# Optimization experiments

Hardware: AMD Instinct MI355X
Metric: run time of the kernel (lower is better)

The kernel has to match this reference:

```python
import jax, jax.numpy as jnp
import numpy as np

B, T = 64, 256
CHAR_V, CHAR_D = 8000, 128
WORD_V, WORD_D = 100000, 300
POS_V, POS_D = 30, 64
SPO_D = 20
D = CHAR_D + WORD_D + POS_D + SPO_D  # 512
L, H, KD, VD, INNER = 4, 8, 64, 64, 2048
C = 25  # num tag classes


def _layer_norm(x, g, b, eps=1e-5):
    m = jnp.mean(x, axis=-1, keepdims=True)
    v = jnp.mean(jnp.square(x - m), axis=-1, keepdims=True)
    return (x - m) * jax.lax.rsqrt(v + eps) * g + b


def setup_inputs() -> dict:
    key = jax.random.key(0)
    ks = jax.random.split(key, 40)
    s = 0.05
    n = lambda k, shp, sc=0.05: jax.random.normal(k, shp, jnp.float32) * sc
    return {
        "char": jax.random.randint(ks[0], (B, T), 0, CHAR_V),
        "word": jax.random.randint(ks[1], (B, T), 0, WORD_V),
        "pos": jax.random.randint(ks[2], (B, T), 0, POS_V),
        "spo": jax.random.normal(ks[3], (B, SPO_D), jnp.float32),
        "seq_len": jax.random.randint(ks[4], (B,), 1, T + 1),
        "tag": jax.random.randint(ks[5], (B, T), 0, C),
        "char_table": n(ks[6], (CHAR_V, CHAR_D)),
        "word_table": n(ks[7], (WORD_V, WORD_D)),
        "pos_table": n(ks[8], (POS_V, POS_D)),
        "ln0_g": jnp.ones((D,), jnp.float32),
        "ln0_b": jnp.zeros((D,), jnp.float32),
        "Wq": n(ks[9], (L, D, H * KD)), "bq": jnp.zeros((L, H * KD), jnp.float32),
        "Wk": n(ks[10], (L, D, H * KD)), "bk": jnp.zeros((L, H * KD), jnp.float32),
        "Wv": n(ks[11], (L, D, H * VD)), "bv": jnp.zeros((L, H * VD), jnp.float32),
        "Wo": n(ks[12], (L, H * VD, D)), "bo": jnp.zeros((L, D), jnp.float32),
        "ln1_g": jnp.ones((L, D), jnp.float32), "ln1_b": jnp.zeros((L, D), jnp.float32),
        "W1": n(ks[13], (L, D, INNER)), "b1": jnp.zeros((L, INNER), jnp.float32),
        "W2": n(ks[14], (L, INNER, D)), "b2": jnp.zeros((L, D), jnp.float32),
        "ln2_g": jnp.ones((L, D), jnp.float32), "ln2_b": jnp.zeros((L, D), jnp.float32),
        "Wout": n(ks[15], (D, C)), "bout": jnp.zeros((C,), jnp.float32),
        "trans": n(ks[16], (C, C)),
    }


def _forward(spo, char_table, word_table, pos_table, ln0_g, ln0_b,
             Wq, bq, Wk, bk, Wv, bv, Wo, bo, ln1_g, ln1_b,
             W1, b1, W2, b2, ln2_g, ln2_b, Wout, bout, trans,
             char, word, pos, seq_len, tag):
    # mask[b,t] = t < seq_len[b]
    mask = (jnp.arange(T)[None, :] < seq_len[:, None]).astype(jnp.float32)  # [B,T]

    # embed + concat + layernorm (dropout in eval mode = identity)
    x = jnp.concatenate([
        char_table[char], word_table[word], pos_table[pos],
        jnp.broadcast_to(spo[:, None, :], (B, T, SPO_D)),
    ], axis=-1)  # [B,T,D]
    x = _layer_norm(x, ln0_g, ln0_b)

    neg_inf = jnp.finfo(x.dtype).min
    key_ok = mask[:, None, None, :] > 0  # [B,1,1,T] key padding mask
    scale = jnp.sqrt(jnp.asarray(KD, x.dtype))
    for l in range(L):
        q = (x @ Wq[l] + bq[l]).reshape(B, T, H, KD).transpose(0, 2, 1, 3)
        k = (x @ Wk[l] + bk[l]).reshape(B, T, H, KD).transpose(0, 2, 1, 3)
        v = (x @ Wv[l] + bv[l]).reshape(B, T, H, VD).transpose(0, 2, 1, 3)
        scores = jnp.einsum('bhqd,bhkd->bhqk', q, k) / scale
        scores = jnp.where(key_ok, scores, neg_inf)
        attn = jax.nn.softmax(scores, axis=-1)
        ctx = jnp.einsum('bhqk,bhkd->bhqd', attn, v).transpose(0, 2, 1, 3).reshape(B, T, H * VD)
        att_out = ctx @ Wo[l] + bo[l]
        h1 = _layer_norm(att_out + x, ln1_g[l], ln1_b[l])
        ff = jax.nn.relu(h1 @ W1[l] + b1[l]) @ W2[l] + b2[l]
        x = _layer_norm(ff + h1, ln2_g[l], ln2_b[l]) * mask[:, :, None]

    logits = x @ Wout + bout  # [B,T,C]

    # ---- CRF negative log likelihood (include_start_end_trans=False) ----
    lg = logits.transpose(1, 0, 2)  # [T,B,C]
    m = mask.T                      # [T,B]

    def step(alpha, inp):
        emit, mt = inp  # emit [B,C], mt [B]
        tmp = alpha[:, :, None] + trans[None, :, :] + emit[:, None, :]  # [B,C,C]
        new = jax.nn.logsumexp(tmp, axis=1)
        alpha = jnp.where(mt[:, None] > 0, new, alpha)
        return alpha, None

    alpha, _ = jax.lax.scan(step, lg[0], (lg[1:], m[1:]))
    log_z = jax.nn.logsumexp(alpha, axis=-1)  # [B]

    tags_t = tag.T  # [T,B]
    emit_gold = jnp.take_along_axis(lg, tags_t[:, :, None], axis=-1)[..., 0] * m  # [T,B]
    trans_gold = trans[tags_t[:-1], tags_t[1:]] * m[1:]  # [T-1,B]
    gold = emit_gold.sum(0) + trans_gold.sum(0)  # [B]

    return jnp.mean(log_z - gold)


def reference(char, word, pos, spo, seq_len, tag, char_table, word_table, pos_table,
              ln0_g, ln0_b, Wq, bq, Wk, bk, Wv, bv, Wo, bo, ln1_g, ln1_b,
              W1, b1, W2, b2, ln2_g, ln2_b, Wout, bout, trans):
    return _forward(spo, char_table, word_table, pos_table, ln0_g, ln0_b,
                    Wq, bq, Wk, bk, Wv, bv, Wo, bo, ln1_g, ln1_b,
                    W1, b1, W2, b2, ln2_g, ln2_b, Wout, bout, trans,
                    char, word, pos, seq_len, tag)
```

## Files before the change

kernel.cpp:

```cpp
#include <hip/hip_runtime.h>
#include <cmath>

namespace {

constexpr int LT = 4;
constexpr int BB = 64;
constexpr int TT = 256;
constexpr int DD = 512;
constexpr int HH = 8;
constexpr int DH = 64;
constexpr int FF = 2048;
constexpr int CC = 25;
constexpr int M_ALL = BB * TT;
constexpr size_t MB = 1024 * 1024;

typedef __attribute__((ext_vector_type(8))) short short8;
typedef __attribute__((ext_vector_type(4))) short short4_;
typedef __attribute__((ext_vector_type(4))) float f32x4;
typedef __attribute__((ext_vector_type(4))) _Float16 half4;

__device__ __forceinline__ float b2f(unsigned short u) {
  union { unsigned int i; float f; } x; x.i = ((unsigned int)u) << 16; return x.f;
}
__device__ __forceinline__ unsigned short f2b(float f) {
  union { float f; unsigned int i; } x; x.f = f;
  unsigned int r = x.i + 0x7FFFu + ((x.i >> 16) & 1u);
  return (unsigned short)(r >> 16);
}
__device__ __forceinline__ float rdlane(float v, int l) {
  union { float f; unsigned int i; } x; x.f = v;
  x.i = (unsigned int)__builtin_amdgcn_readlane((int)x.i, l);
  return x.f;
}
__device__ __forceinline__ void gl_lds16(const void* g, void* l) {
  __builtin_amdgcn_global_load_lds(
      (const __attribute__((address_space(1))) unsigned int*)g,
      (__attribute__((address_space(3))) unsigned int*)l, 16, 0, 0);
}
__device__ __forceinline__ float wredsum(float v) {
#pragma unroll
  for (int o = 32; o > 0; o >>= 1) v += __shfl_xor(v, o, 64);
  return v;
}

__global__ __launch_bounds__(64) void prefix_k(const int* __restrict__ sl,
                                               int* __restrict__ boff) {
  const int l = threadIdx.x;
  int s = sl[l];
#pragma unroll
  for (int o = 1; o < 64; o <<= 1) {
    const int u = __shfl_up(s, o, 64);
    if (l >= o) s += u;
  }
  boff[l + 1] = s;
  if (l == 0) boff[0] = 0;
}

__global__ __launch_bounds__(256) void rowmap_k(const int* __restrict__ sl,
                                                const int* __restrict__ boff,
                                                int* __restrict__ rowmap) {
  const int b = blockIdx.x, t = threadIdx.x;
  if (t < sl[b]) rowmap[boff[b] + t] = (b << 8) | t;
}

__global__ __launch_bounds__(256) void wconv_k(const float* __restrict__ in,
                                               unsigned short* __restrict__ out,
                                               int K, int N, size_t lstride) {
  __shared__ float ts[64][65];
  const int k0 = blockIdx.x * 64, n0 = blockIdx.y * 64;
  in += (size_t)blockIdx.z * K * N;
  out += (size_t)blockIdx.z * lstride;
  const int tid = threadIdx.x;
  for (int i = tid; i < 1024; i += 256) {
    const int r = i >> 4, c4 = i & 15;
    const float4 f = *(const float4*)&in[(size_t)(k0 + r) * N + n0 + c4 * 4];
    ts[r][c4 * 4 + 0] = f.x; ts[r][c4 * 4 + 1] = f.y;
    ts[r][c4 * 4 + 2] = f.z; ts[r][c4 * 4 + 3] = f.w;
  }
  __syncthreads();
  const int n_r = tid >> 2, kc = (tid & 3) * 16;
  short8 v0, v1;
#pragma unroll
  for (int j = 0; j < 8; ++j) {
    v0[j] = (short)f2b(ts[kc + j][n_r]);
    v1[j] = (short)f2b(ts[kc + 8 + j][n_r]);
  }
  unsigned short* op = out + (size_t)(n0 + n_r) * K + k0 + kc;
  *(short8*)op = v0;
  *(short8*)(op + 8) = v1;
}

__global__ __launch_bounds__(256) void embed_ln0_k(
    const int* __restrict__ ch, const int* __restrict__ wd, const int* __restrict__ ps,
    const float* __restrict__ spo, const float* __restrict__ ctab,
    const float* __restrict__ wtab, const float* __restrict__ ptab,
    const float* __restrict__ g, const float* __restrict__ be,
    const int* __restrict__ sl, const int* __restrict__ boff,
    unsigned short* __restrict__ xc) {
  const int row = blockIdx.x * 4 + (threadIdx.x >> 6);
  const int b = row >> 8, t = row & 255;
  if (t >= sl[b]) return;
  const int orow = boff[b] + t;
  const int lane = threadIdx.x & 63;
  const int ci = ch[row], wi = wd[row], pi = ps[row];
  float v[8];
#pragma unroll
  for (int j = 0; j < 2; ++j) {
    const int d = j * 256 + lane * 4;
    float4 f;
    if (d < 128)      f = *(const float4*)&ctab[(size_t)ci * 128 + d];
    else if (d < 428) f = *(const float4*)&wtab[(size_t)wi * 300 + (d - 128)];
    else if (d < 492) f = *(const float4*)&ptab[(size_t)pi * 64 + (d - 428)];
    else              f = *(const float4*)&spo[(size_t)b * 20 + (d - 492)];
    v[j * 4 + 0] = f.x; v[j * 4 + 1] = f.y; v[j * 4 + 2] = f.z; v[j * 4 + 3] = f.w;
  }
  float s = 0.f;
#pragma unroll
  for (int i = 0; i < 8; ++i) s += v[i];
  const float mean = wredsum(s) * (1.0f / 512.0f);
  float vs = 0.f;
#pragma unroll
  for (int i = 0; i < 8; ++i) { const float d = v[i] - mean; vs += d * d; }
  const float rstd = rsqrtf(wredsum(vs) * (1.0f / 512.0f) + 1e-5f);
#pragma unroll
  for (int j = 0; j < 2; ++j) {
    const int d = j * 256 + lane * 4;
    const float4 gv = *(const float4*)&g[d];
    const float4 bv = *(const float4*)&be[d];
    short4_ ob;
    ob[0] = (short)f2b((v[j * 4 + 0] - mean) * rstd * gv.x + bv.x);
    ob[1] = (short)f2b((v[j * 4 + 1] - mean) * rstd * gv.y + bv.y);
    ob[2] = (short)f2b((v[j * 4 + 2] - mean) * rstd * gv.z + bv.z);
    ob[3] = (short)f2b((v[j * 4 + 3] - mean) * rstd * gv.w + bv.w);
    *(short4_*)&xc[(size_t)orow * DD + d] = ob;
  }
}

template <int EPI>
__global__ __launch_bounds__(256) void gemm_mfma(
    const unsigned short* __restrict__ A, const unsigned short* __restrict__ Bt,
    const float* __restrict__ bias, const float* __restrict__ bias2,
    const float* __restrict__ bias3, const unsigned short* __restrict__ res,
    const int* __restrict__ Mptr, const int* __restrict__ rowmap,
    void* __restrict__ outv, void* __restrict__ out2v, void* __restrict__ out3v,
    int M, int N, int K) {
  const int Mp = Mptr[0];
  const int m0 = blockIdx.y * 128, n0 = blockIdx.x * 128;
  if (m0 >= Mp) return;
  __shared__ unsigned short As[2][128 * 64];
  __shared__ unsigned short Bs[2][128 * 64];
  const int tid = threadIdx.x;
  const int wid = tid >> 6, lane = tid & 63;
  const int wr = wid >> 1, wc = wid & 1;
  const int cl = lane & 15, rg = lane >> 4;
  f32x4 acc[4][4];
#pragma unroll
  for (int i = 0; i < 4; ++i)
#pragma unroll
    for (int j = 0; j < 4; ++j) acc[i][j] = (f32x4){0.f, 0.f, 0.f, 0.f};

  const int rbase = tid >> 3, sl = tid & 7;
  const int sc = 8 * (sl ^ (rbase & 7));

  auto stage = [&](int buf, int k0) {
#pragma unroll
    for (int i = 0; i < 4; ++i) {
      const int r = i * 32 + rbase;
      gl_lds16(A + (size_t)(m0 + r) * K + k0 + sc,
               (char*)As[buf] + (i * 256 + tid) * 16);
      gl_lds16(Bt + (size_t)(n0 + r) * K + k0 + sc,
               (char*)Bs[buf] + (i * 256 + tid) * 16);
    }
  };

  stage(0, 0);
  __syncthreads();
  int cur = 0;
  for (int k0 = 0; k0 < K; k0 += 64) {
    if (k0 + 64 < K) stage(cur ^ 1, k0 + 64);
#pragma unroll
    for (int ks = 0; ks < 2; ++ks) {
      short8 a[4], b[4];
      const int kbyte = ks * 64 + rg * 16;
#pragma unroll
      for (int f = 0; f < 4; ++f) {
        const int am = wr * 64 + f * 16 + cl;
        a[f] = *(const short8*)((const char*)As[cur] + am * 128 +
                                (kbyte ^ ((am & 7) << 4)));
        const int bn = wc * 64 + f * 16 + cl;
        b[f] = *(const short8*)((const char*)Bs[cur] + bn * 128 +
                                (kbyte ^ ((bn & 7) << 4)));
      }
#pragma unroll
      for (int mi = 0; mi < 4; ++mi)
#pragma unroll
        for (int ni = 0; ni < 4; ++ni)
          acc[mi][ni] = __builtin_amdgcn_mfma_f32_16x16x32_bf16(a[mi], b[ni],
                                                                acc[mi][ni], 0, 0, 0);
    }
    __syncthreads();
    cur ^= 1;
  }

  int rm[4][4];
  if constexpr (EPI == 5) {
#pragma unroll
    for (int mi = 0; mi < 4; ++mi) {
      const int mb_ = m0 + wr * 64 + mi * 16 + rg * 4;
#pragma unroll
      for (int i = 0; i < 4; ++i)
        rm[mi][i] = (mb_ + i < Mp) ? rowmap[mb_ + i] : -1;
    }
  }

#pragma unroll
  for (int ni = 0; ni < 4; ++ni) {
    const int n = n0 + wc * 64 + ni * 16 + cl;
    float bv;
    if constexpr (EPI == 5) {
      bv = (n < 512) ? bias[n] : (n < 1024 ? bias2[n - 512] : bias3[n - 1024]);
    } else {
      bv = bias[n];
    }
#pragma unroll
    for (int mi = 0; mi < 4; ++mi) {
      if constexpr (EPI == 5) {
        const int hh = (n >> 6) & 7, d = n & 63;
        if (n < 1024) {
          unsigned short* outp = (unsigned short*)((n < 512) ? outv : out2v);
#pragma unroll
          for (int i = 0; i < 4; ++i) {
            const int rmv = rm[mi][i];
            if (rmv >= 0) {
              const int bb = rmv >> 8, tt = rmv & 255;
              outp[(((size_t)(bb * HH + hh) * TT + tt) << 6) + d] =
                  f2b(acc[mi][ni][i] + bv);
            }
          }
        } else {
          const int rm0 = rm[mi][0];
          if (rm0 >= 0 && rm[mi][3] == rm0 + 3) {
            half4 pk;
#pragma unroll
            for (int i = 0; i < 4; ++i) pk[i] = (_Float16)(acc[mi][ni][i] + bv);
            *(half4*)((_Float16*)out3v +
                      ((((size_t)((rm0 >> 8) * HH + hh) * DH + d) << 8) + (rm0 & 255))) = pk;
          } else {
#pragma unroll
            for (int i = 0; i < 4; ++i) {
              const int rmv = rm[mi][i];
              if (rmv >= 0)
                ((_Float16*)out3v)[(((size_t)((rmv >> 8) * HH + hh) * DH + d) << 8) +
                                   (rmv & 255)] = (_Float16)(acc[mi][ni][i] + bv);
            }
          }
        }
      } else {
#pragma unroll
        for (int i = 0; i < 4; ++i) {
          const int m = m0 + wr * 64 + mi * 16 + rg * 4 + i;
          const float v = acc[mi][ni][i] + bv;
          if constexpr (EPI == 1) {
            ((unsigned short*)outv)[(size_t)m * N + n] = f2b(fmaxf(v, 0.f));
          } else if constexpr (EPI == 7) {
            ((unsigned short*)outv)[(size_t)m * N + n] =
                f2b(v + b2f(res[(size_t)m * N + n]));
          }
        }
      }
    }
  }
}

__global__ __launch_bounds__(256) void attn_mfma_k(
    const unsigned short* __restrict__ qb, const unsigned short* __restrict__ kbp,
    const _Float16* __restrict__ vtp, const int* __restrict__ seq_len,
    const int* __restrict__ boff, unsigned short* __restrict__ cb) {
  __shared__ unsigned short Ks[256 * 64];
  __shared__ _Float16 Vs[64 * 256];
  __shared__ unsigned short Os[64 * 64];
  const int bh = blockIdx.x;
  const int b = bh >> 3, h = bh & 7;
  const int tid = threadIdx.x;
  const int wid = tid >> 6, lane = tid & 63;
  const int cl = lane & 15, rg = lane >> 4;
  const int len = seq_len[b];
  const int off = boff[b];

  {
    const int r = tid >> 3, sl = tid & 7;
#pragma unroll
    for (int i = 0; i < 8; ++i) {
      if (i * 32 < len) {
        const int row = i * 32 + r;
        gl_lds16(kbp + ((size_t)bh * TT + row) * DH + 8 * (sl ^ (row & 7)),
                 (char*)Ks + (i * 256 + tid) * 16);
      }
    }
#pragma unroll
    for (int i = 0; i < 8; ++i) {
      const int u = i * 256 + tid;
      const int vrow = u >> 5, vsl = u & 31;
      gl_lds16(vtp + ((size_t)bh * DH + vrow) * TT + 8 * (vsl ^ (vrow & 7)),
               (char*)Vs + u * 16);
    }
  }
  __syncthreads();

  for (int qt4 = 0; qt4 < 4; ++qt4) {
    if (qt4 * 64 >= len) break;
    f32x4 o[4];
#pragma unroll
    for (int db = 0; db < 4; ++db) o[db] = (f32x4){0.f, 0.f, 0.f, 0.f};
    {
      const int q0 = qt4 * 64 + wid * 16;
      short8 bqf[2];
      const unsigned short* qp = qb + ((size_t)bh * TT + q0 + cl) * DH + rg * 8;
      bqf[0] = *(const short8*)qp;
      bqf[1] = *(const short8*)(qp + 32);
      f32x4 s[16];
#pragma unroll
      for (int kk = 0; kk < 16; ++kk) {
        s[kk] = (f32x4){0.f, 0.f, 0.f, 0.f};
        if (kk * 16 < len) {
          const int row = kk * 16 + cl;
          const char* base = (const char*)Ks + row * 128;
          const int sw = (row & 7) << 4;
          const short8 a0 = *(const short8*)(base + ((rg * 16) ^ sw));
          const short8 a1 = *(const short8*)(base + ((64 + rg * 16) ^ sw));
          s[kk] = __builtin_amdgcn_mfma_f32_16x16x32_bf16(a0, bqf[0], s[kk], 0, 0, 0);
          s[kk] = __builtin_amdgcn_mfma_f32_16x16x32_bf16(a1, bqf[1], s[kk], 0, 0, 0);
        }
      }
      float mx = -3.0e38f;
#pragma unroll
      for (int kk = 0; kk < 16; ++kk)
        if (kk * 16 < len) {
#pragma unroll
          for (int i = 0; i < 4; ++i) {
            float v = s[kk][i] * 0.125f;
            v = (kk * 16 + rg * 4 + i < len) ? v : -3.0e38f;
            s[kk][i] = v;
            mx = fmaxf(mx, v);
          }
        }
      mx = fmaxf(mx, __shfl_xor(mx, 16, 64));
      mx = fmaxf(mx, __shfl_xor(mx, 32, 64));
      float lsum = 0.f;
#pragma unroll
      for (int kk = 0; kk < 16; ++kk)
        if (kk * 16 < len) {
#pragma unroll
          for (int i = 0; i < 4; ++i) {
            const float p = __expf(s[kk][i] - mx);
            s[kk][i] = p;
            lsum += p;
          }
        }
      lsum += __shfl_xor(lsum, 16, 64);
      lsum += __shfl_xor(lsum, 32, 64);
      const float rl = 1.0f / lsum;
#pragma unroll
      for (int kk = 0; kk < 16; ++kk)
        if (kk * 16 < len) {
          half4 bp;
#pragma unroll
          for (int i = 0; i < 4; ++i) bp[i] = (_Float16)(s[kk][i] * rl);
#pragma unroll
          for (int db = 0; db < 4; ++db) {
            const int vrow = db * 16 + cl;
            const int byte = kk * 32 + rg * 8;
            const half4 a = *(const half4*)((const char*)Vs + vrow * 512 +
                              ((byte & ~15) ^ ((vrow & 7) << 4)) + (byte & 15));
            o[db] = __builtin_amdgcn_mfma_f32_16x16x16f16(a, bp, o[db], 0, 0, 0);
          }
        }
    }
    __syncthreads();
    {
      const int orow = wid * 16 + cl;
      char* obase = (char*)Os + orow * 128;
      const int sw = (orow & 7) << 4;
#pragma unroll
      for (int db = 0; db < 4; ++db) {
        short4_ pk;
#pragma unroll
        for (int i = 0; i < 4; ++i) pk[i] = (short)f2b(o[db][i]);
        const int byte = db * 32 + rg * 8;
        *(short4_*)(obase + ((byte & ~15) ^ sw) + (byte & 15)) = pk;
      }
    }
    __syncthreads();
    {
      const int r = tid >> 2, part = tid & 3;
      const int t = qt4 * 64 + r;
      if (t < len) {
        const int sw = (r & 7) << 4;
        const char* rbase = (const char*)Os + r * 128;
        const short8 w0 = *(const short8*)(rbase + ((part * 32) ^ sw));
        const short8 w1 = *(const short8*)(rbase + ((part * 32 + 16) ^ sw));
        unsigned short* dst = cb + ((size_t)(off + t)) * DD + h * DH + part * 16;
        *(short8*)dst = w0;
        *(short8*)(dst + 8) = w1;
      }
    }
  }
}

__global__ __launch_bounds__(256) void ln_k(const unsigned short* __restrict__ a,
                                            const float* __restrict__ g,
                                            const float* __restrict__ be,
                                            const int* __restrict__ Mptr,
                                            unsigned short* __restrict__ outb) {
  const int row = blockIdx.x * 4 + (threadIdx.x >> 6);
  if (row >= Mptr[0]) return;
  const int lane = threadIdx.x & 63;
  float v[8];
  {
    const short8 va = *(const short8*)&a[(size_t)row * DD + lane * 8];
#pragma unroll
    for (int i = 0; i < 8; ++i) v[i] = b2f((unsigned short)va[i]);
  }
  float s = 0.f;
#pragma unroll
  for (int i = 0; i < 8; ++i) s += v[i];
  const float mean = wredsum(s) * (1.0f / 512.0f);
  float vs = 0.f;
#pragma unroll
  for (int i = 0; i < 8; ++i) { const float d = v[i] - mean; vs += d * d; }
  const float rstd = rsqrtf(wredsum(vs) * (1.0f / 512.0f) + 1e-5f);
  const float4 g0 = *(const float4*)&g[lane * 8];
  const float4 g1 = *(const float4*)&g[lane * 8 + 4];
  const float4 b0 = *(const float4*)&be[lane * 8];
  const float4 b1 = *(const float4*)&be[lane * 8 + 4];
  const float gg[8] = {g0.x, g0.y, g0.z, g0.w, g1.x, g1.y, g1.z, g1.w};
  const float bb[8] = {b0.x, b0.y, b0.z, b0.w, b1.x, b1.y, b1.z, b1.w};
  short8 ob;
#pragma unroll
  for (int i = 0; i < 8; ++i)
    ob[i] = (short)f2b((v[i] - mean) * rstd * gg[i] + bb[i]);
  *(short8*)&outb[(size_t)row * DD + lane * 8] = ob;
}

__global__ __launch_bounds__(256) void logits_k(const unsigned short* __restrict__ xb,
                                                const float* __restrict__ W,
                                                const float* __restrict__ bo,
                                                const int* __restrict__ Mptr,
                                                float* __restrict__ lg) {
  const int r0 = blockIdx.x * 8;
  if (r0 >= Mptr[0]) return;
  __shared__ float xs[8][516];
  for (int i = threadIdx.x; i < 512; i += 256) {
    const int rr = i >> 6, c8 = (i & 63) * 8;
    const short8 v = *(const short8*)&xb[(size_t)(r0 + rr) * DD + c8];
#pragma unroll
    for (int j = 0; j < 8; ++j) xs[rr][c8 + j] = b2f((unsigned short)v[j]);
  }
  __syncthreads();
  const int r = threadIdx.x >> 5, c = threadIdx.x & 31;
  if (c < CC) {
    float acc = 0.f;
#pragma unroll 8
    for (int k = 0; k < DD; ++k) acc += xs[r][k] * W[k * CC + c];
    lg[(size_t)(r0 + r) * CC + c] = acc + bo[c];
  }
}

__global__ __launch_bounds__(64) void crf_k(const float* __restrict__ lg,
                                            const int* __restrict__ tag,
                                            const int* __restrict__ seq_len,
                                            const int* __restrict__ boff,
                                            const float* __restrict__ trans,
                                            float* __restrict__ nll) {
  __shared__ float eexp[TT * CC + 64];
  __shared__ float tr[CC * CC];
  const int b = blockIdx.x;
  const int l = threadIdx.x;
  const int len = seq_len[b];
  const float* lgb = lg + (size_t)boff[b] * CC;
  for (int i = l; i < len * CC; i += 64) eexp[i] = __expf(lgb[i]);
  for (int i = l; i < CC * CC; i += 64) tr[i] = trans[i];
  __syncthreads();
  const int lc = (l < CC) ? l : (CC - 1);
  float et[CC];
#pragma unroll
  for (int i = 0; i < CC; ++i) et[i] = __expf(tr[i * CC + lc]);
  const float e00 = lgb[0];
  float M = e00;
  float A = (l < CC) ? __expf(lgb[l] - e00) : 0.f;
  for (int t = 1; t < len; ++t) {
    const float e = eexp[t * CC + lc];
    float s0 = 0.f, s1 = 0.f, s2 = 0.f, s3 = 0.f, s4 = 0.f;
#pragma unroll
    for (int i = 0; i < CC; i += 5) {
      s0 += rdlane(A, i + 0) * et[i + 0];
      s1 += rdlane(A, i + 1) * et[i + 1];
      s2 += rdlane(A, i + 2) * et[i + 2];
      s3 += rdlane(A, i + 3) * et[i + 3];
      s4 += rdlane(A, i + 4) * et[i + 4];
    }
    A = (((s0 + s1) + (s2 + s3)) + s4) * e;
    if ((t & 3) == 0) {
      const float r = rdlane(A, 0);
      M += __logf(r);
      A *= __builtin_amdgcn_rcpf(r);
    }
  }
  const float tot = wredsum((l < CC) ? A : 0.f);
  float gold = 0.f;
  for (int t = l; t < len; t += 64)
    gold += lgb[t * CC + tag[b * TT + t]];
  for (int t = 1 + l; t < len; t += 64)
    gold += tr[tag[b * TT + t - 1] * CC + tag[b * TT + t]];
  gold = wredsum(gold);
  if (l == 0) nll[b] = (M + __logf(tot)) - gold;
}

__global__ __launch_bounds__(64) void final_k(const float* __restrict__ nll,
                                              float* __restrict__ out) {
  float v = nll[threadIdx.x];
  v = wredsum(v);
  if (threadIdx.x == 0) out[0] = v * (1.0f / 64.0f);
}

}

extern "C" void kernel_launch(void* const* d_in, const int* in_sizes, int n_in,
                              void* d_out, int out_size, void* d_ws, size_t ws_size,
                              hipStream_t stream) {
  (void)in_sizes; (void)n_in; (void)out_size; (void)ws_size;
  const int* chi = (const int*)d_in[0];
  const int* wdi = (const int*)d_in[1];
  const int* psi = (const int*)d_in[2];
  const float* spo = (const float*)d_in[3];
  const int* seq_len = (const int*)d_in[4];
  const int* tag = (const int*)d_in[5];
  const float* ctab = (const float*)d_in[6];
  const float* wtab = (const float*)d_in[7];
  const float* ptab = (const float*)d_in[8];
  const float* ln0g = (const float*)d_in[9];
  const float* ln0b = (const float*)d_in[10];
  const float* Wq = (const float*)d_in[11];
  const float* bq = (const float*)d_in[12];
  const float* Wk = (const float*)d_in[13];
  const float* bk = (const float*)d_in[14];
  const float* Wv = (const float*)d_in[15];
  const float* bv = (const float*)d_in[16];
  const float* Wo = (const float*)d_in[17];
  const float* bo = (const float*)d_in[18];
  const float* ln1g = (const float*)d_in[19];
  const float* ln1b = (const float*)d_in[20];
  const float* W1 = (const float*)d_in[21];
  const float* b1 = (const float*)d_in[22];
  const float* W2 = (const float*)d_in[23];
  const float* b2 = (const float*)d_in[24];
  const float* ln2g = (const float*)d_in[25];
  const float* ln2b = (const float*)d_in[26];
  const float* Wout = (const float*)d_in[27];
  const float* bout = (const float*)d_in[28];
  const float* trans = (const float*)d_in[29];

  char* w8 = (char*)d_ws;
  unsigned short* ib  = (unsigned short*)(w8);
  unsigned short* xc  = (unsigned short*)(w8 + 64 * MB);
  unsigned short* cbx = (unsigned short*)(w8 + 80 * MB);
  unsigned short* ab  = (unsigned short*)(w8 + 96 * MB);
  unsigned short* hb  = (unsigned short*)(w8 + 112 * MB);
  unsigned short* t0b = (unsigned short*)(w8 + 128 * MB);
  unsigned short* qbuf = (unsigned short*)(w8 + 144 * MB);
  unsigned short* kbuf = (unsigned short*)(w8 + 160 * MB);
  _Float16* vtb = (_Float16*)(w8 + 176 * MB);
  unsigned short* wqkv = (unsigned short*)(w8 + 192 * MB);
  unsigned short* wot = (unsigned short*)(w8 + 198 * MB);
  unsigned short* w1t = (unsigned short*)(w8 + 200 * MB);
  unsigned short* w2t = (unsigned short*)(w8 + 208 * MB);
  float* lg = (float*)(w8 + 216 * MB);
  float* nll = (float*)(w8 + 218 * MB);
  int* boff = (int*)(w8 + 219 * MB);
  int* rowmap = (int*)(w8 + 220 * MB);
  const int* Mptr = boff + 64;

  prefix_k<<<1, 64, 0, stream>>>(seq_len, boff);
  rowmap_k<<<BB, 256, 0, stream>>>(seq_len, boff, rowmap);

  const size_t QKVS = (size_t)1536 * 512;
  wconv_k<<<dim3(8, 8, LT), 256, 0, stream>>>(Wq, wqkv, DD, DD, QKVS);
  wconv_k<<<dim3(8, 8, LT), 256, 0, stream>>>(Wk, wqkv + 512 * 512, DD, DD, QKVS);
  wconv_k<<<dim3(8, 8, LT), 256, 0, stream>>>(Wv, wqkv + 1024 * 512, DD, DD, QKVS);
  wconv_k<<<dim3(8, 8, LT), 256, 0, stream>>>(Wo, wot, DD, DD, (size_t)DD * DD);
  wconv_k<<<dim3(8, 32, LT), 256, 0, stream>>>(W1, w1t, DD, FF, (size_t)DD * FF);
  wconv_k<<<dim3(32, 8, LT), 256, 0, stream>>>(W2, w2t, FF, DD, (size_t)FF * DD);

  embed_ln0_k<<<M_ALL / 4, 256, 0, stream>>>(chi, wdi, psi, spo, ctab, wtab, ptab,
                                             ln0g, ln0b, seq_len, boff, xc);

  for (int l = 0; l < LT; ++l) {
    gemm_mfma<5><<<dim3(12, 128), 256, 0, stream>>>(
        xc, wqkv + (size_t)l * QKVS, bq + l * DD, bk + l * DD, bv + l * DD,
        nullptr, Mptr, rowmap, qbuf, kbuf, vtb, M_ALL, 1536, DD);
    attn_mfma_k<<<BB * HH, 256, 0, stream>>>(qbuf, kbuf, vtb, seq_len, boff, cbx);
    gemm_mfma<7><<<dim3(4, 128), 256, 0, stream>>>(
        cbx, wot + (size_t)l * DD * DD, bo + l * DD, nullptr, nullptr,
        xc, Mptr, nullptr, ab, nullptr, nullptr, M_ALL, DD, DD);
    ln_k<<<M_ALL / 4, 256, 0, stream>>>(ab, ln1g + l * DD, ln1b + l * DD, Mptr, hb);
    gemm_mfma<1><<<dim3(FF / 128, 128), 256, 0, stream>>>(
        hb, w1t + (size_t)l * FF * DD, b1 + l * FF, nullptr, nullptr,
        nullptr, Mptr, nullptr, ib, nullptr, nullptr, M_ALL, FF, DD);
    gemm_mfma<7><<<dim3(DD / 128, 128), 256, 0, stream>>>(
        ib, w2t + (size_t)l * FF * DD, b2 + l * DD, nullptr, nullptr,
        hb, Mptr, nullptr, t0b, nullptr, nullptr, M_ALL, DD, FF);
    ln_k<<<M_ALL / 4, 256, 0, stream>>>(t0b, ln2g + l * DD, ln2b + l * DD, Mptr, xc);
  }
  logits_k<<<M_ALL / 8, 256, 0, stream>>>(xc, Wout, bout, Mptr, lg);
  crf_k<<<BB, 64, 0, stream>>>(lg, tag, seq_len, boff, trans, nll);
  final_k<<<1, 64, 0, stream>>>(nll, (float*)d_out);
}
```

Baseline: 814.8 us.

## Load GEMM B operand directly to registers, remap workgroups, merge QKV weight conversion

The GEMM kernel stops staging the B (weight) tile through LDS. Each wave instead reads its B fragments straight from global memory into registers every k-step, which halves LDS usage and removes LDS writes and reads for B. Workgroup IDs are also remapped so that consecutive blocks are spread across XCDs, and the three Q/K/V weight conversions are merged into one launch. The trade-off is that B loads are now uncoalesced-ish per-lane global reads, are exposed without double buffering, and B tiles are re-read by both wave rows.

```diff
diff --git a/kernel.cpp b/kernel.cpp
--- a/kernel.cpp
+++ b/kernel.cpp
@@ -63,13 +63,25 @@
   if (t < sl[b]) rowmap[boff[b] + t] = (b << 8) | t;
 }
 
-__global__ __launch_bounds__(256) void wconv_k(const float* __restrict__ in,
+template <int NSRC>
+__global__ __launch_bounds__(256) void wconv_k(const float* __restrict__ in0,
+                                               const float* __restrict__ in1,
+                                               const float* __restrict__ in2,
                                                unsigned short* __restrict__ out,
-                                               int K, int N, size_t lstride) {
+                                               int K, int N, size_t lstride,
+                                               size_t sstride) {
   __shared__ float ts[64][65];
   const int k0 = blockIdx.x * 64, n0 = blockIdx.y * 64;
-  in += (size_t)blockIdx.z * K * N;
-  out += (size_t)blockIdx.z * lstride;
+  const float* in = in0;
+  if constexpr (NSRC == 3) {
+    const int s = blockIdx.z / LT;
+    in = (s == 0) ? in0 : (s == 1 ? in1 : in2);
+    in += (size_t)(blockIdx.z % LT) * K * N;
+    out += (size_t)(blockIdx.z % LT) * lstride + (size_t)(blockIdx.z / LT) * sstride;
+  } else {
+    in += (size_t)blockIdx.z * K * N;
+    out += (size_t)blockIdx.z * lstride;
+  }
   const int tid = threadIdx.x;
   for (int i = tid; i < 1024; i += 256) {
     const int r = i >> 4, c4 = i & 15;
@@ -145,10 +157,16 @@
     void* __restrict__ outv, void* __restrict__ out2v, void* __restrict__ out3v,
     int M, int N, int K) {
   const int Mp = Mptr[0];
-  const int m0 = blockIdx.y * 128, n0 = blockIdx.x * 128;
+  const int nx = gridDim.x;
+  {
+  }
+  int flat = blockIdx.y * nx + blockIdx.x;
+  const int nwg = nx * gridDim.y;
+  flat = (flat & 7) * (nwg >> 3) + (flat >> 3);
+  const int bx = flat % nx, by = flat / nx;
+  const int m0 = by * 128, n0 = bx * 128;
   if (m0 >= Mp) return;
   __shared__ unsigned short As[2][128 * 64];
-  __shared__ unsigned short Bs[2][128 * 64];
   const int tid = threadIdx.x;
   const int wid = tid >> 6, lane = tid & 63;
   const int wr = wid >> 1, wc = wid & 1;
@@ -162,40 +180,43 @@
   const int rbase = tid >> 3, sl = tid & 7;
   const int sc = 8 * (sl ^ (rbase & 7));
 
-  auto stage = [&](int buf, int k0) {
+  auto stageA = [&](int buf, int k0) {
 #pragma unroll
     for (int i = 0; i < 4; ++i) {
       const int r = i * 32 + rbase;
       gl_lds16(A + (size_t)(m0 + r) * K + k0 + sc,
                (char*)As[buf] + (i * 256 + tid) * 16);
-      gl_lds16(Bt + (size_t)(n0 + r) * K + k0 + sc,
-               (char*)Bs[buf] + (i * 256 + tid) * 16);
     }
   };
 
-  stage(0, 0);
+  const unsigned short* bp = Bt + (size_t)(n0 + wc * 64 + cl) * K + rg * 8;
+
+  stageA(0, 0);
   __syncthreads();
   int cur = 0;
   for (int k0 = 0; k0 < K; k0 += 64) {
-    if (k0 + 64 < K) stage(cur ^ 1, k0 + 64);
+    if (k0 + 64 < K) stageA(cur ^ 1, k0 + 64);
+    short8 b[2][4];
+#pragma unroll
+    for (int ks = 0; ks < 2; ++ks)
+#pragma unroll
+      for (int f = 0; f < 4; ++f)
+        b[ks][f] = *(const short8*)(bp + (size_t)(f * 16) * K + k0 + ks * 32);
 #pragma unroll
     for (int ks = 0; ks < 2; ++ks) {
-      short8 a[4], b[4];
+      short8 a[4];
       const int kbyte = ks * 64 + rg * 16;
 #pragma unroll
       for (int f = 0; f < 4; ++f) {
         const int am = wr * 64 + f * 16 + cl;
         a[f] = *(const short8*)((const char*)As[cur] + am * 128 +
                                 (kbyte ^ ((am & 7) << 4)));
-        const int bn = wc * 64 + f * 16 + cl;
-        b[f] = *(const short8*)((const char*)Bs[cur] + bn * 128 +
-                                (kbyte ^ ((bn & 7) << 4)));
       }
 #pragma unroll
       for (int mi = 0; mi < 4; ++mi)
 #pragma unroll
         for (int ni = 0; ni < 4; ++ni)
-          acc[mi][ni] = __builtin_amdgcn_mfma_f32_16x16x32_bf16(a[mi], b[ni],
+          acc[mi][ni] = __builtin_amdgcn_mfma_f32_16x16x32_bf16(a[mi], b[ks][ni],
                                                                 acc[mi][ni], 0, 0, 0);
     }
     __syncthreads();
@@ -584,12 +605,14 @@
   rowmap_k<<<BB, 256, 0, stream>>>(seq_len, boff, rowmap);
 
   const size_t QKVS = (size_t)1536 * 512;
-  wconv_k<<<dim3(8, 8, LT), 256, 0, stream>>>(Wq, wqkv, DD, DD, QKVS);
-  wconv_k<<<dim3(8, 8, LT), 256, 0, stream>>>(Wk, wqkv + 512 * 512, DD, DD, QKVS);
-  wconv_k<<<dim3(8, 8, LT), 256, 0, stream>>>(Wv, wqkv + 1024 * 512, DD, DD, QKVS);
-  wconv_k<<<dim3(8, 8, LT), 256, 0, stream>>>(Wo, wot, DD, DD, (size_t)DD * DD);
-  wconv_k<<<dim3(8, 32, LT), 256, 0, stream>>>(W1, w1t, DD, FF, (size_t)DD * FF);
-  wconv_k<<<dim3(32, 8, LT), 256, 0, stream>>>(W2, w2t, FF, DD, (size_t)FF * DD);
+  wconv_k<3><<<dim3(8, 8, 3 * LT), 256, 0, stream>>>(
+      Wq, Wk, Wv, wqkv, DD, DD, QKVS, (size_t)512 * 512);
+  wconv_k<1><<<dim3(8, 8, LT), 256, 0, stream>>>(
+      Wo, nullptr, nullptr, wot, DD, DD, (size_t)DD * DD, 0);
+  wconv_k<1><<<dim3(8, 32, LT), 256, 0, stream>>>(
+      W1, nullptr, nullptr, w1t, DD, FF, (size_t)DD * FF, 0);
+  wconv_k<1><<<dim3(32, 8, LT), 256, 0, stream>>>(
+      W2, nullptr, nullptr, w2t, FF, DD, (size_t)FF * DD, 0);
 
   embed_ln0_k<<<M_ALL / 4, 256, 0, stream>>>(chi, wdi, psi, spo, ctab, wtab, ptab,
                                              ln0g, ln0b, seq_len, boff, xc);
```

Result: slower. 1.381 ms (+69.5%).
